# Performance work log

Hardware: AMD Instinct MI355X
Metric: run time of the kernel (lower is better)

## Reference

```python
import jax, jax.numpy as jnp
import numpy as np

B, T_IN, T_OUT, D, M, N = 4, 10, 5, 5, 96, 96
H1 = 64      # hidden dim of deep ConvLSTM layers
ATTN = 32    # attention bottleneck channels
SEL = 0      # selected_dim


def _conv(x, w, b):
    # SAME conv, NCHW / OIHW
    p = (w.shape[-1] - 1) // 2
    y = jax.lax.conv_general_dilated(x, w, (1, 1), [(p, p), (p, p)],
                                     dimension_numbers=('NCHW', 'OIHW', 'NCHW'))
    return y + b[None, :, None, None]


def _cell(xt, h, c, w, b):
    # standard ConvLSTM cell (no peephole): conv over concat(x, h) -> i,f,o,g
    z = _conv(jnp.concatenate([xt, h], axis=1), w, b)
    i, f, o, g = jnp.split(z, 4, axis=1)
    c = jax.nn.sigmoid(f) * c + jax.nn.sigmoid(i) * jnp.tanh(g)
    h = jax.nn.sigmoid(o) * jnp.tanh(c)
    return h, c


def setup_inputs() -> dict:
    key = jax.random.key(0)
    ks = jax.random.split(key, 12)
    w = lambda k, s: jax.random.normal(k, s, jnp.float32) * 0.05
    z = lambda n: jnp.zeros((n,), jnp.float32)
    return {
        'x': jax.random.normal(ks[0], (B, T_IN, D, M, N), jnp.float32),
        # encoder ConvLSTM cells: hidden dims [1, H1, H1]
        'enc_w0': w(ks[1], (4 * 1, D + 1, 3, 3)), 'enc_b0': z(4 * 1),
        'enc_w1': w(ks[2], (4 * H1, 1 + H1, 3, 3)), 'enc_b1': z(4 * H1),
        'enc_w2': w(ks[3], (4 * H1, H1 + H1, 3, 3)), 'enc_b2': z(4 * H1),
        # decoder ConvLSTM cells: hidden dims [H1, H1, 1]
        'dec_w0': w(ks[4], (4 * H1, 1 + H1, 3, 3)), 'dec_b0': z(4 * H1),
        'dec_w1': w(ks[5], (4 * H1, H1 + H1, 3, 3)), 'dec_b1': z(4 * H1),
        'dec_w2': w(ks[6], (4 * 1, H1 + 1, 3, 3)), 'dec_b2': z(4 * 1),
        # input attention (DA-RNN style with convs): e_k = v(tanh(Wi*x_k + Wh*[h;c]))
        'attn_wi': w(ks[7], (ATTN, T_IN, 3, 3)), 'attn_bi': z(ATTN),
        'attn_wh': w(ks[8], (ATTN, 2, 3, 3)), 'attn_bh': z(ATTN),
        'attn_wv': w(ks[9], (1, ATTN, 3, 3)), 'attn_bv': z(1),
        # temporal_cnn: Conv2d(1 + window_in, 1, kernel_size=1) + ReLU
        'tcnn_w': w(ks[10], (1, T_IN + 1, 1, 1)), 'tcnn_b': z(1),
    }


def reference(x, enc_w0, enc_b0, enc_w1, enc_b1, enc_w2, enc_b2,
              dec_w0, dec_b0, dec_w1, dec_b1, dec_w2, dec_b2,
              attn_wi, attn_bi, attn_wh, attn_bh, attn_wv, attn_bv,
              tcnn_w, tcnn_b):
    b = x.shape[0]

    def attn_reweight(xs, h, c):
        # xs: (b, t, d, m, n); hidden term shared across the d channels
        hid_e = _conv(jnp.concatenate([h, c], axis=1), attn_wh, attn_bh)
        def per_k(xk):  # (b, t, m, n): time-as-channels
            e = jnp.tanh(_conv(xk, attn_wi, attn_bi) + hid_e)
            return _conv(e, attn_wv, attn_bv)[:, 0]  # (b, m, n)
        alpha = jax.vmap(per_k, in_axes=2, out_axes=1)(xs)  # (b, d, m, n)
        ea = jnp.exp(alpha)
        return xs * (ea / jnp.max(ea))[:, None]  # global-max normalization

    def run_layer(xs, h, c, w, bb):
        def step(carry, xt):
            hh, cc = _cell(xt, carry[0], carry[1], w, bb)
            return (hh, cc), hh
        (h, c), hs = jax.lax.scan(step, (h, c), jnp.swapaxes(xs, 0, 1))
        return jnp.swapaxes(hs, 0, 1), (h, c)

    # ---------- encoder ----------
    h0 = jnp.zeros((b, 1, M, N), x.dtype); c0 = jnp.zeros_like(h0)
    def enc0_step(carry, t):
        xs, h, c = carry
        xs = attn_reweight(xs, h, c)  # re-weight whole sequence each step
        xt = jax.lax.dynamic_index_in_dim(xs, t, axis=1, keepdims=False)
        h, c = _cell(xt, h, c, enc_w0, enc_b0)
        return (xs, h, c), h
    (_, h0, c0), hs0 = jax.lax.scan(enc0_step, (x, h0, c0), jnp.arange(T_IN))
    out0 = jnp.swapaxes(hs0, 0, 1)  # (b, T_IN, 1, m, n)

    h1 = jnp.zeros((b, H1, M, N), x.dtype); c1 = jnp.zeros_like(h1)
    out1, (h1, c1) = run_layer(out0, h1, c1, enc_w1, enc_b1)
    h2 = jnp.zeros((b, H1, M, N), x.dtype); c2 = jnp.zeros_like(h2)
    out2, (h2, c2) = run_layer(out1, h2, c2, enc_w2, enc_b2)

    # ---------- decoder (encoder states reversed) ----------
    dec_in = jnp.zeros((b, T_OUT, 1, M, N), x.dtype)
    d0, _ = run_layer(dec_in, h2, c2, dec_w0, dec_b0)
    d1, _ = run_layer(d0, h1, c1, dec_w1, dec_b1)

    y_prev = x[:, :, SEL]  # (b, T_IN, m, n): selected variable, time-as-channels
    def dec2_step(carry, xt):
        h, c, yp = carry
        h, c = _cell(xt, h, c, dec_w2, dec_b2)          # (b, 1, m, n)
        ycat = jnp.concatenate([yp, h], axis=1)         # (b, T_IN+1, m, n)
        h = jax.nn.relu(_conv(ycat, tcnn_w, tcnn_b))    # temporal 1x1 CNN readout
        return (h, c, ycat[:, 1:]), h
    _, hs = jax.lax.scan(dec2_step, (h0, c0, y_prev), jnp.swapaxes(d1, 0, 1))
    return jnp.swapaxes(hs, 0, 1)  # (b, T_OUT, 1, m, n)
```

## Files before the change

kernel.cpp:

```cpp
#include <hip/hip_runtime.h>


#define PIX  9216
#define NB   4
#define TIN  10
#define TOUT 5
#define ND   5
#define HID  64

typedef __attribute__((ext_vector_type(8))) short bf16x8;
typedef __attribute__((ext_vector_type(4))) float f32x4;

__device__ __forceinline__ float sigmf_(float x) { return 1.0f / (1.0f + __expf(-x)); }
__device__ __forceinline__ float tanhf_(float x) { return 1.0f - 2.0f / (__expf(2.0f * x) + 1.0f); }
__device__ __forceinline__ unsigned short f2bf(float f) {
    unsigned u = __float_as_uint(f);
    unsigned r = u + 0x7FFFu + ((u >> 16) & 1u);
    return (unsigned short)(r >> 16);
}
__device__ __forceinline__ float bf2f(unsigned short u) {
    return __uint_as_float(((unsigned)u) << 16);
}
__device__ __forceinline__ unsigned fmap_(float f) {
    unsigned u = __float_as_uint(f);
    return (u & 0x80000000u) ? ~u : (u | 0x80000000u);
}
__device__ __forceinline__ float funmap_(unsigned v) {
    return __uint_as_float((v & 0x80000000u) ? (v ^ 0x80000000u) : ~v);
}
__device__ __forceinline__ void gload_lds16(const void* g, void* l) {
    __builtin_amdgcn_global_load_lds(
        (const __attribute__((address_space(1))) void*)g,
        (__attribute__((address_space(3))) void*)l, 16, 0, 0);
}

template <int NCH>
__device__ __forceinline__ void
cell64_body(char* smem, int bid,
            const unsigned short* __restrict__ inP,
            const unsigned short* __restrict__ wP,
            const float* __restrict__ bias,
            const float* cprev, float* cout,
            const float* __restrict__ zeropg,
            unsigned short* __restrict__ d1, int d1_coff, int d1_ncg,
            unsigned short* __restrict__ d2, int d2_coff, int d2_ncg)
{
    const int lane = threadIdx.x;
    const int wv   = threadIdx.y;
    const int tid  = wv * 64 + lane;
    const int rid = (bid & 7) * 48 + (bid >> 3);
    const int y = rid % 96, b = rid / 96;
    const int l15 = lane & 15, l4 = lane >> 4;
    const int NCG = NCH * 4;

    const int scg  = tid & 3;
    const int spr0 = tid >> 2;

    auto stage = [&](char* buf, int cc) {
#pragma unroll
        for (int i = 0; i < 5; ++i) {
            int pr = spr0 + i * 64;
            int r = pr / 98;
            int p = pr - r * 98;
            int gy = y - 1 + r, gx = p - 1;
            const void* g = (const void*)zeropg;
            if (pr < 294 && (unsigned)gy < 96u && (unsigned)gx < 96u) {
                int cg = scg ^ ((p >> 1) & 3);
                g = (const void*)(inP + (((size_t)(b * NCG + cc * 4 + cg) * 9216
                                          + gy * 96 + gx) << 3));
            }
            gload_lds16(g, buf + i * 4096 + wv * 1024);
        }
    };

    f32x4 acc[4][6] = {};
    bf16x8 af[2][4];

#pragma unroll
    for (int g = 0; g < 4; ++g)
        af[0][g] = *(const bf16x8*)(wP
            + ((size_t)(0 * NCH + 0) * 256 + g * 64 + wv * 16 + l15) * 32 + l4 * 8);

    stage(smem, 0);
    __syncthreads();
#pragma unroll
    for (int cc = 0; cc < NCH; ++cc) {
        if (cc + 1 < NCH) stage(smem + ((cc + 1) & 1) * 20480, cc + 1);
        const char* buf = smem + (cc & 1) * 20480;
#pragma unroll
        for (int tap = 0; tap < 9; ++tap) {
            const int T = cc * 9 + tap;
            if (T + 1 < NCH * 9) {
                const int cc2 = (T + 1) / 9, tap2 = (T + 1) % 9;
#pragma unroll
                for (int g = 0; g < 4; ++g)
                    af[(T + 1) & 1][g] = *(const bf16x8*)(wP
                        + ((size_t)(tap2 * NCH + cc2) * 256 + g * 64 + wv * 16 + l15) * 32 + l4 * 8);
            }
            const int ky = tap / 3, kx = tap % 3;
            bf16x8 bk[6];
#pragma unroll
            for (int k = 0; k < 6; ++k) {
                int p = k * 16 + kx + l15;
                int slot = l4 ^ ((p >> 1) & 3);
                bk[k] = *(const bf16x8*)(buf + (ky * 98 + p) * 64 + slot * 16);
            }
            __builtin_amdgcn_s_setprio(1);
#pragma unroll
            for (int g = 0; g < 4; ++g)
#pragma unroll
                for (int k = 0; k < 6; ++k)
                    acc[g][k] = __builtin_amdgcn_mfma_f32_16x16x32_bf16(
                        af[T & 1][g], bk[k], acc[g][k], 0, 0, 0);
            __builtin_amdgcn_s_setprio(0);
        }
        if (cc + 1 < NCH) __syncthreads();
    }

#pragma unroll
    for (int r = 0; r < 4; ++r) {
        int hc = wv * 16 + l4 * 4 + r;
        float bi = bias[hc], bff = bias[64 + hc];
        float bo = bias[128 + hc], bg = bias[192 + hc];
#pragma unroll
        for (int k = 0; k < 6; ++k) {
            int px = k * 16 + l15;
            int gpix = y * 96 + px;
            float ii = sigmf_(acc[0][k][r] + bi);
            float ff = sigmf_(acc[1][k][r] + bff);
            float oo = sigmf_(acc[2][k][r] + bo);
            float gg = tanhf_(acc[3][k][r] + bg);
            int cidx = (b * HID + hc) * 9216 + gpix;
            float cn = ff * cprev[cidx] + ii * gg;
            cout[cidx] = cn;
            unsigned short hb = f2bf(oo * tanhf_(cn));
            int ch1 = d1_coff + hc;
            d1[((size_t)(b * d1_ncg + (ch1 >> 3)) * 9216 + gpix) * 8 + (ch1 & 7)] = hb;
            if (d2) {
                int ch2 = d2_coff + hc;
                d2[((size_t)(b * d2_ncg + (ch2 >> 3)) * 9216 + gpix) * 8 + (ch2 & 7)] = hb;
            }
        }
    }
}

__device__ __forceinline__ void
attnE_body(char* smem, int aid,
           const unsigned short* __restrict__ xsp, const unsigned short* __restrict__ wiP,
           const float* __restrict__ h0, const float* __restrict__ c0,
           const float* __restrict__ wh, const float* __restrict__ bh,
           const float* __restrict__ bi, unsigned short* __restrict__ eP)
{
    float* heS = (float*)smem;
    const int lane = threadIdx.x, wvid = threadIdx.y;
    const int tile = aid % 36, k = (aid / 36) % 5, bb = aid / 180;
    const int l15 = lane & 15, l4 = lane >> 4;
    const int tid = wvid * 64 + lane;

    {
        int p = tile * 256 + tid;
        int y = p / 96, x = p - y * 96;
        float hv9[9], cv9[9];
        const float* hp = h0 + bb * PIX;
        const float* cp = c0 + bb * PIX;
#pragma unroll
        for (int t9 = 0; t9 < 9; ++t9) {
            int gy = y + t9 / 3 - 1, gx = x + t9 % 3 - 1;
            bool ok = (unsigned)gy < 96u && (unsigned)gx < 96u;
            hv9[t9] = ok ? hp[gy * 96 + gx] : 0.0f;
            cv9[t9] = ok ? cp[gy * 96 + gx] : 0.0f;
        }
#pragma unroll
        for (int ch = 0; ch < 32; ++ch) {
            float a = bi[ch] + bh[ch];
#pragma unroll
            for (int t9 = 0; t9 < 9; ++t9) {
                a = fmaf(wh[(ch * 2 + 0) * 9 + t9], hv9[t9], a);
                a = fmaf(wh[(ch * 2 + 1) * 9 + t9], cv9[t9], a);
            }
            heS[tid * 33 + ch] = a;
        }
    }

    bf16x8 af[5][2];
#pragma unroll
    for (int j = 0; j < 5; ++j)
#pragma unroll
        for (int m = 0; m < 2; ++m)
            af[j][m] = *(const bf16x8*)(wiP + ((size_t)(j * 32 + m * 16 + l15)) * 32 + l4 * 8);

    const unsigned short* xb = xsp + (size_t)(bb * ND + k) * PIX * 16;
    const int p0 = tile * 256 + wvid * 64;

    f32x4 acc[4][2] = {};
#pragma unroll
    for (int nf = 0; nf < 4; ++nf) {
        int p = p0 + nf * 16 + l15;
        int y = p / 96, x = p - y * 96;
#pragma unroll
        for (int j = 0; j < 5; ++j) {
            int tp = 2 * j + (l4 >> 1);
            bf16x8 bk = { 0, 0, 0, 0, 0, 0, 0, 0 };
            if (tp < 9) {
                int gy = y + tp / 3 - 1, gx = x + tp % 3 - 1;
                if ((unsigned)gy < 96u && (unsigned)gx < 96u)
                    bk = *(const bf16x8*)(xb + ((size_t)(gy * 96 + gx)) * 16 + (l4 & 1) * 8);
            }
            acc[nf][0] = __builtin_amdgcn_mfma_f32_16x16x32_bf16(af[j][0], bk, acc[nf][0], 0, 0, 0);
            acc[nf][1] = __builtin_amdgcn_mfma_f32_16x16x32_bf16(af[j][1], bk, acc[nf][1], 0, 0, 0);
        }
    }

    __syncthreads();

#pragma unroll
    for (int nf = 0; nf < 4; ++nf) {
        int p = p0 + nf * 16 + l15;
        int pl = wvid * 64 + nf * 16 + l15;
        const float* hrow = &heS[pl * 33];
#pragma unroll
        for (int m = 0; m < 2; ++m) {
            ushort4 o;
            o.x = f2bf(tanhf_(acc[nf][m][0] + hrow[m * 16 + l4 * 4 + 0]));
            o.y = f2bf(tanhf_(acc[nf][m][1] + hrow[m * 16 + l4 * 4 + 1]));
            o.z = f2bf(tanhf_(acc[nf][m][2] + hrow[m * 16 + l4 * 4 + 2]));
            o.w = f2bf(tanhf_(acc[nf][m][3] + hrow[m * 16 + l4 * 4 + 3]));
            *(ushort4*)(eP + ((size_t)(bb * ND + k) * PIX + p) * 32 + m * 16 + l4 * 4) = o;
        }
    }
}

__device__ __forceinline__ void
alpha_body(char* smem, int aid,
           const unsigned short* __restrict__ eP, const float* __restrict__ wvv,
           const float* __restrict__ bv, float* __restrict__ alpha,
           unsigned* __restrict__ msl)
{
    const int tid = threadIdx.y * 64 + threadIdx.x;
    const int tile = aid % 36, k = (aid / 36) % 5, bb = aid / 180;
    int p = tile * 256 + tid;
    int y = p / 96, x = p - y * 96;
    const unsigned short* eb = eP + (size_t)(bb * ND + k) * PIX * 32;
    float acc = bv[0];
#pragma unroll
    for (int ky = 0; ky < 3; ++ky) {
        int gy = y + ky - 1;
        if ((unsigned)gy >= 96u) continue;
#pragma unroll
        for (int kx = 0; kx < 3; ++kx) {
            int gx = x + kx - 1;
            if ((unsigned)gx >= 96u) continue;
            int tap = ky * 3 + kx;
            const unsigned short* ee = eb + ((size_t)(gy * 96 + gx)) * 32;
#pragma unroll
            for (int cg = 0; cg < 4; ++cg) {
                bf16x8 ev = *(const bf16x8*)(ee + cg * 8);
#pragma unroll
                for (int jj = 0; jj < 8; ++jj)
                    acc = fmaf(wvv[(cg * 8 + jj) * 9 + tap], bf2f((unsigned short)ev[jj]), acc);
            }
        }
    }
    alpha[(size_t)(bb * ND + k) * PIX + p] = acc;

    float* s = (float*)smem;
    s[tid] = acc;
    __syncthreads();
    for (int st = 128; st > 0; st >>= 1) {
        if (tid < st) s[tid] = fmaxf(s[tid], s[tid + st]);
        __syncthreads();
    }
    if (tid == 0) atomicMax(msl, fmap_(s[0]));
}

__device__ __forceinline__ void
dec2_body(int did,
          const unsigned short* __restrict__ inP, int ncg, int cgbase,
          const float* __restrict__ hprev, const float* cprev,
          const unsigned short* __restrict__ wm, const float* __restrict__ w2,
          const float* __restrict__ bias,
          const float* __restrict__ tw, const float* __restrict__ tb,
          const float* __restrict__ yprev,
          float* __restrict__ ynext, float* __restrict__ hcarry,
          float* __restrict__ outp, float* cout)
{
    const int wv = threadIdx.y, lane = threadIdx.x;
    const int l15 = lane & 15, l4 = lane >> 4;
    const int bx = did % 144, b = did / 144;
    const int p0 = (bx * 4 + wv) * 16;
    const int y = p0 / 96, xbase = p0 - y * 96;
    const int x = xbase + l15;

    f32x4 acc = {0.f, 0.f, 0.f, 0.f};
#pragma unroll
    for (int ky = 0; ky < 3; ++ky) {
        int gy = y + ky - 1;
        bool oky = (unsigned)gy < 96u;
#pragma unroll
        for (int kx = 0; kx < 3; ++kx) {
            const int tap = ky * 3 + kx;
            int gx = x + kx - 1;
            bool ok = oky && ((unsigned)gx < 96u);
#pragma unroll
            for (int cc = 0; cc < 2; ++cc) {
                bf16x8 a = *(const bf16x8*)(wm + ((size_t)(tap * 2 + cc) * 16 + l15) * 32 + l4 * 8);
                bf16x8 bk = { 0, 0, 0, 0, 0, 0, 0, 0 };
                if (ok)
                    bk = *(const bf16x8*)(inP + ((size_t)(b * ncg + cgbase + cc * 4 + l4) * 9216
                                                 + gy * 96 + gx) * 8);
                acc = __builtin_amdgcn_mfma_f32_16x16x32_bf16(a, bk, acc, 0, 0, 0);
            }
        }
    }

    if (l4 == 0) {
        int px = p0 + l15;
        float aI = acc[0] + bias[0];
        float aF = acc[1] + bias[1];
        float aO = acc[2] + bias[2];
        float aG = acc[3] + bias[3];
        const float* hp = hprev + b * PIX;
#pragma unroll
        for (int ky = 0; ky < 3; ++ky) {
            int gy = y + ky - 1;
            if ((unsigned)gy >= 96u) continue;
#pragma unroll
            for (int kx = 0; kx < 3; ++kx) {
                int gx = x + kx - 1;
                if ((unsigned)gx >= 96u) continue;
                int tap = ky * 3 + kx;
                float hv = hp[gy * 96 + gx];
                aI = fmaf(w2[(0 * 65 + 64) * 9 + tap], hv, aI);
                aF = fmaf(w2[(1 * 65 + 64) * 9 + tap], hv, aF);
                aO = fmaf(w2[(2 * 65 + 64) * 9 + tap], hv, aO);
                aG = fmaf(w2[(3 * 65 + 64) * 9 + tap], hv, aG);
            }
        }
        int idx = b * PIX + px;
        float cn = sigmf_(aF) * cprev[idx] + sigmf_(aI) * tanhf_(aG);
        cout[idx] = cn;
        float h = sigmf_(aO) * tanhf_(cn);

        float a2 = tb[0];
#pragma unroll
        for (int c2 = 0; c2 < TIN; ++c2)
            a2 = fmaf(tw[c2], yprev[(size_t)(b * TIN + c2) * PIX + px], a2);
        a2 = fmaf(tw[TIN], h, a2);
        float o = fmaxf(a2, 0.0f);
        outp[(size_t)b * TOUT * PIX + px] = o;
#pragma unroll
        for (int c2 = 0; c2 < TIN - 1; ++c2)
            ynext[(size_t)(b * TIN + c2) * PIX + px] = yprev[(size_t)(b * TIN + c2 + 1) * PIX + px];
        ynext[(size_t)(b * TIN + 9) * PIX + px] = h;
        hcarry[idx] = o;
    }
}

template <int NCH, bool ATTN>
__global__ void __launch_bounds__(256, 2)
mk_cell_attnE(const unsigned short* __restrict__ inP, const unsigned short* __restrict__ wP,
              const float* __restrict__ bias, const float* cprev, float* cout,
              const float* __restrict__ zeropg,
              unsigned short* __restrict__ d1, int d1_coff, int d1_ncg,
              unsigned short* __restrict__ d2, int d2_coff, int d2_ncg,
              const unsigned short* __restrict__ xsp, const unsigned short* __restrict__ wiP,
              const float* __restrict__ h0, const float* __restrict__ c0,
              const float* __restrict__ wh, const float* __restrict__ bh,
              const float* __restrict__ bi, unsigned short* __restrict__ eP)
{
    __shared__ __align__(16) char smem[40960];
    if (blockIdx.x < 384)
        cell64_body<NCH>(smem, blockIdx.x, inP, wP, bias, cprev, cout, zeropg,
                         d1, d1_coff, d1_ncg, d2, d2_coff, d2_ncg);
    else if (ATTN)
        attnE_body(smem, blockIdx.x - 384, xsp, wiP, h0, c0, wh, bh, bi, eP);
}

template <int NCH, bool ATTN>
__global__ void __launch_bounds__(256, 2)
mk_cell_alpha(const unsigned short* __restrict__ inP, const unsigned short* __restrict__ wP,
              const float* __restrict__ bias, const float* cprev, float* cout,
              const float* __restrict__ zeropg,
              unsigned short* __restrict__ d1, int d1_coff, int d1_ncg,
              unsigned short* __restrict__ d2, int d2_coff, int d2_ncg,
              const unsigned short* __restrict__ eP, const float* __restrict__ wvv,
              const float* __restrict__ bv, float* __restrict__ alpha,
              unsigned* __restrict__ msl)
{
    __shared__ __align__(16) char smem[40960];
    if (blockIdx.x < 384)
        cell64_body<NCH>(smem, blockIdx.x, inP, wP, bias, cprev, cout, zeropg,
                         d1, d1_coff, d1_ncg, d2, d2_coff, d2_ncg);
    else if (ATTN)
        alpha_body(smem, blockIdx.x - 384, eP, wvv, bv, alpha, msl);
}

template <bool HAS0, bool HAS2>
__global__ void __launch_bounds__(256, 2)
mk_dec(const unsigned short* __restrict__ d1in, const unsigned short* __restrict__ wpd1,
       const float* __restrict__ b1, float* c1, unsigned short* __restrict__ d1out,
       const float* __restrict__ zeropg,
       const unsigned short* __restrict__ d0in, const unsigned short* __restrict__ wpd0,
       const float* __restrict__ b0, float* c2, unsigned short* __restrict__ d0out,
       unsigned short* __restrict__ d1next,
       const unsigned short* __restrict__ d2in,
       const float* __restrict__ hprev, float* c0,
       const unsigned short* __restrict__ wd2m, const float* __restrict__ w2,
       const float* __restrict__ b2,
       const float* __restrict__ tw, const float* __restrict__ tb,
       const float* __restrict__ yprev, float* __restrict__ ynext,
       float* __restrict__ hcarry, float* __restrict__ outp)
{
    __shared__ __align__(16) char smem[40960];
    if (blockIdx.x < 384) {
        cell64_body<4>(smem, blockIdx.x, d1in, wpd1, b1, c1, c1, zeropg,
                       d1out, 64, 16, nullptr, 0, 0);
    } else if (blockIdx.x < 768) {
        if (HAS0)
            cell64_body<2>(smem, blockIdx.x - 384, d0in, wpd0, b0, c2, c2, zeropg,
                           d0out, 0, 8, d1next, 0, 16);
    } else {
        if (HAS2)
            dec2_body(blockIdx.x - 768, d2in, 16, 8, hprev, c0, wd2m, w2, b2,
                      tw, tb, yprev, ynext, hcarry, outp, c0);
    }
}

template <int NCH>
__global__ void __launch_bounds__(256, 2)
cell_k(const unsigned short* __restrict__ inP, const unsigned short* __restrict__ wP,
       const float* __restrict__ bias, const float* cprev, float* cout,
       const float* __restrict__ zeropg,
       unsigned short* __restrict__ d1, int d1_coff, int d1_ncg,
       unsigned short* __restrict__ d2, int d2_coff, int d2_ncg)
{
    __shared__ __align__(16) char smem[40960];
    cell64_body<NCH>(smem, blockIdx.x, inP, wP, bias, cprev, cout, zeropg,
                     d1, d1_coff, d1_ncg, d2, d2_coff, d2_ncg);
}

__global__ void __launch_bounds__(256)
dec2_k(const unsigned short* __restrict__ d2in, const float* __restrict__ hprev,
       float* c0, const unsigned short* __restrict__ wd2m, const float* __restrict__ w2,
       const float* __restrict__ b2, const float* __restrict__ tw, const float* __restrict__ tb,
       const float* __restrict__ yprev, float* __restrict__ ynext,
       float* __restrict__ hcarry, float* __restrict__ outp)
{
    dec2_body(blockIdx.x, d2in, 16, 8, hprev, c0, wd2m, w2, b2,
              tw, tb, yprev, ynext, hcarry, outp, c0);
}

__global__ void __launch_bounds__(256)
attn_e_k(const unsigned short* __restrict__ xsp, const unsigned short* __restrict__ wiP,
         const float* __restrict__ h0, const float* __restrict__ c0,
         const float* __restrict__ wh, const float* __restrict__ bh,
         const float* __restrict__ bi, unsigned short* __restrict__ eP)
{
    __shared__ __align__(16) char smem[33792];
    attnE_body(smem, blockIdx.x, xsp, wiP, h0, c0, wh, bh, bi, eP);
}

__global__ void __launch_bounds__(256)
alpha_k(const unsigned short* __restrict__ eP, const float* __restrict__ wvv,
        const float* __restrict__ bv, float* __restrict__ alpha, unsigned* __restrict__ msl)
{
    __shared__ __align__(16) char smem[1024];
    alpha_body(smem, blockIdx.x, eP, wvv, bv, alpha, msl);
}

__global__ void __launch_bounds__(256)
prep_kernel(const float* __restrict__ enc_w1, const float* __restrict__ enc_w2,
            const float* __restrict__ dec_w0, const float* __restrict__ dec_w1,
            const float* __restrict__ dec_w2, const float* __restrict__ attn_wi,
            const float* __restrict__ x,
            unsigned short* __restrict__ wpe1, unsigned short* __restrict__ wpe2,
            unsigned short* __restrict__ wpd0, unsigned short* __restrict__ wpd1,
            unsigned short* __restrict__ wd2m, unsigned short* __restrict__ wiP,
            unsigned short* __restrict__ xsp, float* __restrict__ yp)
{
    int gid = blockIdx.x;
    auto wpack = [&](const float* w, unsigned short* wp, int WCIN, int NCH,
                     int coff, int climit, int base) {
        int idx = (gid - base) * 256 + threadIdx.x;
        if (idx >= 9 * NCH * 256 * 32) return;
        int k = idx & 31;
        int ocp = (idx >> 5) & 255;
        int rest = idx >> 13;
        int cc = rest % NCH, tap = rest / NCH;
        int hc = ocp >> 2, gate = ocp & 3;
        int c = cc * 32 + k;
        float v = 0.0f;
        if (c < climit) v = w[((gate * 64 + hc) * WCIN + (c + coff)) * 9 + tap];
        wp[idx] = f2bf(v);
    };
    if (gid < 864) { wpack(enc_w1, wpe1, 65, 3, 0, 65, 0); return; }
    if (gid < 2016) { wpack(enc_w2, wpe2, 128, 4, 0, 128, 864); return; }
    if (gid < 2592) { wpack(dec_w0, wpd0, 65, 2, 1, 64, 2016); return; }
    if (gid < 3744) { wpack(dec_w1, wpd1, 128, 4, 0, 128, 2592); return; }
    if (gid < 3780) {
        int idx = (gid - 3744) * 256 + threadIdx.x;
        if (idx < 9 * 2 * 16 * 32) {
            int k = idx & 31;
            int oc = (idx >> 5) & 15;
            int cc = (idx >> 9) & 1;
            int tap = idx >> 10;
            float v = 0.0f;
            if (oc < 4) v = dec_w2[(oc * 65 + cc * 32 + k) * 9 + tap];
            wd2m[idx] = f2bf(v);
        }
        return;
    }
    if (gid < 3800) {
        int idx = (gid - 3780) * 256 + threadIdx.x;
        if (idx < 5120) {
            int kl = idx & 31, oc = (idx >> 5) & 31, j = idx >> 10;
            int tappos = kl >> 4, ch = kl & 15;
            int tap = 2 * j + tappos;
            float v = 0.0f;
            if (tap < 9 && ch < 10) v = attn_wi[(oc * TIN + ch) * 9 + tap];
            wiP[idx] = f2bf(v);
        }
        return;
    }
    if (gid < 4520) {
        int idx = (gid - 3800) * 256 + threadIdx.x;
        int p = idx % PIX;
        int q = idx / PIX;
        int d = q % ND, bb = q / ND;
        unsigned short tmp[16];
#pragma unroll
        for (int t = 0; t < TIN; ++t)
            tmp[t] = f2bf(x[((size_t)(bb * TIN + t) * ND + d) * PIX + p]);
#pragma unroll
        for (int t = TIN; t < 16; ++t) tmp[t] = 0;
        uint4* dst = (uint4*)(xsp + (size_t)idx * 16);
        dst[0] = *(uint4*)&tmp[0];
        dst[1] = *(uint4*)&tmp[8];
        return;
    }
    {
        int idx = (gid - 4520) * 256 + threadIdx.x;
        int p = idx % PIX;
        int q = idx / PIX;
        yp[idx] = x[(size_t)(q * ND + 0) * PIX + p];
    }
}


__global__ void __launch_bounds__(256)
small_cell5(const float* __restrict__ xs_t,
            const float* __restrict__ hprev, const float* cprev,
            const float* __restrict__ w, const float* __restrict__ bias,
            float* __restrict__ hout, float* cout,
            unsigned short* __restrict__ pk, int ncg)
{
    __shared__ float z[4][64];
    const int pxl = threadIdx.x & 63, gate = threadIdx.x >> 6;
    const int p = blockIdx.x * 64 + pxl, bb = blockIdx.y;
    const int y = p / 96, x = p - y * 96;
    float acc = bias[gate];
#pragma unroll
    for (int cin = 0; cin < 6; ++cin) {
        const float* src = (cin < 5) ? (xs_t + (bb * TIN * ND + cin) * PIX)
                                     : (hprev + bb * PIX);
        const float* wp = w + (gate * 6 + cin) * 9;
#pragma unroll
        for (int ky = 0; ky < 3; ++ky) {
            int gy = y + ky - 1;
            if ((unsigned)gy >= 96u) continue;
#pragma unroll
            for (int kx = 0; kx < 3; ++kx) {
                int gx = x + kx - 1;
                if ((unsigned)gx >= 96u) continue;
                acc = fmaf(wp[ky * 3 + kx], src[gy * 96 + gx], acc);
            }
        }
    }
    z[gate][pxl] = acc;
    __syncthreads();
    if (threadIdx.x < 64) {
        int pp = blockIdx.x * 64 + threadIdx.x;
        int idx = bb * PIX + pp;
        float cn = sigmf_(z[1][threadIdx.x]) * cprev[idx]
                 + sigmf_(z[0][threadIdx.x]) * tanhf_(z[3][threadIdx.x]);
        cout[idx] = cn;
        float h = sigmf_(z[2][threadIdx.x]) * tanhf_(cn);
        hout[idx] = h;
        pk[((size_t)(bb * ncg) * 9216 + pp) * 8] = f2bf(h);
    }
}

__global__ void scale_pack_kernel(float* __restrict__ xs, unsigned short* __restrict__ xsp,
                                  const float* __restrict__ alpha,
                                  const unsigned* __restrict__ msl)
{
    int idx = blockIdx.x * 256 + threadIdx.x;
    int p = idx % PIX;
    int q = idx / PIX;
    int d = q % ND, bb = q / ND;
    float mval = funmap_(msl[0]);
    float w = __expf(alpha[idx] - mval);
    unsigned short tmp[16];
#pragma unroll
    for (int t = 0; t < TIN; ++t) {
        size_t xi = ((size_t)(bb * TIN + t) * ND + d) * PIX + p;
        float v = xs[xi] * w;
        xs[xi] = v;
        tmp[t] = f2bf(v);
    }
#pragma unroll
    for (int t = TIN; t < 16; ++t) tmp[t] = 0;
    uint4* dst = (uint4*)(xsp + (size_t)idx * 16);
    dst[0] = *(uint4*)&tmp[0];
    dst[1] = *(uint4*)&tmp[8];
}

extern "C" void kernel_launch(void* const* d_in, const int* in_sizes, int n_in,
                              void* d_out, int out_size, void* d_ws, size_t ws_size,
                              hipStream_t stream)
{
    const float* x       = (const float*)d_in[0];
    const float* enc_w0  = (const float*)d_in[1];
    const float* enc_b0  = (const float*)d_in[2];
    const float* enc_w1  = (const float*)d_in[3];
    const float* enc_b1  = (const float*)d_in[4];
    const float* enc_w2  = (const float*)d_in[5];
    const float* enc_b2  = (const float*)d_in[6];
    const float* dec_w0  = (const float*)d_in[7];
    const float* dec_b0  = (const float*)d_in[8];
    const float* dec_w1  = (const float*)d_in[9];
    const float* dec_b1  = (const float*)d_in[10];
    const float* dec_w2  = (const float*)d_in[11];
    const float* dec_b2  = (const float*)d_in[12];
    const float* attn_wi = (const float*)d_in[13];
    const float* attn_bi = (const float*)d_in[14];
    const float* attn_wh = (const float*)d_in[15];
    const float* attn_bh = (const float*)d_in[16];
    const float* attn_wv = (const float*)d_in[17];
    const float* attn_bv = (const float*)d_in[18];
    const float* tcnn_w  = (const float*)d_in[19];
    const float* tcnn_b  = (const float*)d_in[20];
    float* out = (float*)d_out;

    char* cur = (char*)d_ws;
    auto alloc = [&](size_t bytes) { char* p = cur; cur += (bytes + 255) & ~(size_t)255; return p; };
    float* xs   = (float*)alloc((size_t)NB * TIN * ND * PIX * 4);
    float* alp  = (float*)alloc((size_t)NB * ND * PIX * 4);
    float* ypa  = (float*)alloc((size_t)NB * TIN * PIX * 4);
    float* ypb  = (float*)alloc((size_t)NB * TIN * PIX * 4);
    unsigned short* wpe1 = (unsigned short*)alloc((size_t)9 * 3 * 256 * 32 * 2);
    unsigned short* wpe2 = (unsigned short*)alloc((size_t)9 * 4 * 256 * 32 * 2);
    unsigned short* wpd0 = (unsigned short*)alloc((size_t)9 * 2 * 256 * 32 * 2);
    unsigned short* wpd1 = (unsigned short*)alloc((size_t)9 * 4 * 256 * 32 * 2);
    unsigned short* wd2m = (unsigned short*)alloc((size_t)9 * 2 * 16 * 32 * 2);
    unsigned short* xsp  = (unsigned short*)alloc((size_t)NB * ND * PIX * 16 * 2);
    unsigned short* wiP  = (unsigned short*)alloc(5120 * 2);
    unsigned short* eP   = (unsigned short*)alloc((size_t)NB * ND * PIX * 32 * 2);
    char* zbeg = cur;
    float* h0a  = (float*)alloc(NB * PIX * 4);
    float* h0b  = (float*)alloc(NB * PIX * 4);
    float* c0   = (float*)alloc(NB * PIX * 4);
    float* c1   = (float*)alloc((size_t)NB * HID * PIX * 4);
    float* c2   = (float*)alloc((size_t)NB * HID * PIX * 4);
    const size_t IN1_B = (size_t)NB * 12 * PIX * 8 * 2;
    const size_t IN2_B = (size_t)NB * 16 * PIX * 8 * 2;
    unsigned short* In1a = (unsigned short*)alloc(IN1_B);
    unsigned short* In1b = (unsigned short*)alloc(IN1_B);
    unsigned short* In2a = (unsigned short*)alloc(IN2_B);
    unsigned short* In2b = (unsigned short*)alloc(IN2_B);
    unsigned* mslot = (unsigned*)alloc(256);
    float* zeropg = (float*)alloc(256);
    char* zend = cur;

    hipMemcpyAsync(xs, x, (size_t)NB * TIN * ND * PIX * 4, hipMemcpyDeviceToDevice, stream);
    hipMemsetAsync(zbeg, 0, (size_t)(zend - zbeg), stream);
    prep_kernel<<<dim3(5960), 256, 0, stream>>>(enc_w1, enc_w2, dec_w0, dec_w1, dec_w2,
                                                attn_wi, x, wpe1, wpe2, wpd0, wpd1,
                                                wd2m, wiP, xsp, ypa);

    dim3 blk(64, 4);
    float *h0 = h0a, *h0n = h0b;
    unsigned short *i1c = In1a, *i1n = In1b, *i2c = In2a, *i2n = In2b;

    attn_e_k<<<dim3(720), blk, 0, stream>>>(xsp, wiP, h0, c0, attn_wh, attn_bh, attn_bi, eP);
    alpha_k<<<dim3(720), blk, 0, stream>>>(eP, attn_wv, attn_bv, alp, mslot + 0);
    scale_pack_kernel<<<dim3(720), 256, 0, stream>>>(xs, xsp, alp, mslot + 0);
    small_cell5<<<dim3(144, NB), 256, 0, stream>>>(xs + 0, h0, c0, enc_w0, enc_b0,
                                                   h0n, c0, i1c, 12);
    { float* tmp = h0; h0 = h0n; h0n = tmp; }

    for (int t = 0; t < TIN; ++t) {
        const bool hn = (t < TIN - 1);
        unsigned short* e1d1 = hn ? i1n : In2a;
        int e1o = hn ? 1 : 64;
        int e1n = hn ? 12 : 16;
        unsigned short* e2d1 = hn ? i2n : In1a;
        int e2o = hn ? 64 : 0;
        int e2n = hn ? 16 : 8;
        int grid = 384 + (hn ? 720 : 0);

        if (hn)
            mk_cell_attnE<3, true><<<dim3(grid), blk, 0, stream>>>(
                i1c, wpe1, enc_b1, c1, c1, zeropg, e1d1, e1o, e1n, i2c, 0, 16,
                xsp, wiP, h0, c0, attn_wh, attn_bh, attn_bi, eP);
        else
            mk_cell_attnE<3, false><<<dim3(grid), blk, 0, stream>>>(
                i1c, wpe1, enc_b1, c1, c1, zeropg, e1d1, e1o, e1n, i2c, 0, 16,
                xsp, wiP, h0, c0, attn_wh, attn_bh, attn_bi, eP);

        if (hn)
            mk_cell_alpha<4, true><<<dim3(grid), blk, 0, stream>>>(
                i2c, wpe2, enc_b2, c2, c2, zeropg, e2d1, e2o, e2n, nullptr, 0, 0,
                eP, attn_wv, attn_bv, alp, mslot + t + 1);
        else
            mk_cell_alpha<4, false><<<dim3(grid), blk, 0, stream>>>(
                i2c, wpe2, enc_b2, c2, c2, zeropg, e2d1, e2o, e2n, nullptr, 0, 0,
                eP, attn_wv, attn_bv, alp, mslot + t + 1);

        if (hn) {
            scale_pack_kernel<<<dim3(720), 256, 0, stream>>>(xs, xsp, alp, mslot + t + 1);
            small_cell5<<<dim3(144, NB), 256, 0, stream>>>(xs + (size_t)(t + 1) * ND * PIX,
                                                           h0, c0, enc_w0, enc_b0,
                                                           h0n, c0, i1n, 12);
            { float* tmp = h0; h0 = h0n; h0n = tmp; }
        }
        { unsigned short* tmp = i1c; i1c = i1n; i1n = tmp; }
        { unsigned short* tmp = i2c; i2c = i2n; i2n = tmp; }
    }

    float *hc = h0, *hcn = h0n;
    cell_k<2><<<dim3(384), blk, 0, stream>>>(In1a, wpd0, dec_b0, c2, c2, zeropg,
                                             In1b, 0, 8, In2a, 0, 16);
    mk_dec<true, false><<<dim3(768), blk, 0, stream>>>(
        In2a, wpd1, dec_b1, c1, In2b, zeropg,
        In1b, wpd0, dec_b0, c2, In1a, In2b,
        nullptr, nullptr, nullptr, nullptr, nullptr, nullptr, nullptr, nullptr,
        nullptr, nullptr, nullptr, nullptr);
    mk_dec<true, true><<<dim3(1344), blk, 0, stream>>>(
        In2b, wpd1, dec_b1, c1, In2a, zeropg,
        In1a, wpd0, dec_b0, c2, In1b, In2a,
        In2b, hc, c0, wd2m, dec_w2, dec_b2, tcnn_w, tcnn_b,
        ypa, ypb, hcn, out + 0 * PIX);
    mk_dec<true, true><<<dim3(1344), blk, 0, stream>>>(
        In2a, wpd1, dec_b1, c1, In2b, zeropg,
        In1b, wpd0, dec_b0, c2, In1a, In2b,
        In2a, hcn, c0, wd2m, dec_w2, dec_b2, tcnn_w, tcnn_b,
        ypb, ypa, hc, out + 1 * PIX);
    mk_dec<true, true><<<dim3(1344), blk, 0, stream>>>(
        In2b, wpd1, dec_b1, c1, In2a, zeropg,
        In1a, wpd0, dec_b0, c2, In1b, In2a,
        In2b, hc, c0, wd2m, dec_w2, dec_b2, tcnn_w, tcnn_b,
        ypa, ypb, hcn, out + 2 * PIX);
    mk_dec<false, true><<<dim3(1344), blk, 0, stream>>>(
        In2a, wpd1, dec_b1, c1, In2b, zeropg,
        nullptr, nullptr, nullptr, nullptr, nullptr, nullptr,
        In2a, hcn, c0, wd2m, dec_w2, dec_b2, tcnn_w, tcnn_b,
        ypb, ypa, hc, out + 3 * PIX);
    dec2_k<<<dim3(576), blk, 0, stream>>>(In2b, hc, c0, wd2m, dec_w2, dec_b2,
                                          tcnn_w, tcnn_b, ypa, ypb, hcn, out + 4 * PIX);
}
```

Baseline: 1.285 ms.

## Fuse attention scaling with first ConvLSTM cell and deepen weight prefetch

Merges the attention-weighted input scaling/packing kernel and the layer-0 ConvLSTM cell into a single launch. Input buffers are ping-ponged so the cell blocks can recompute the scaled input from the unscaled copy without waiting on the scaling blocks. The MFMA conv loop also prefetches weight fragments two taps ahead using a triple buffer instead of one tap ahead. The aim is to cut launch and serialization overhead per timestep and hide weight-load latency, at the cost of redundant exp computations, extra workspace and more registers.

```diff
diff --git a/kernel.cpp b/kernel.cpp
--- a/kernel.cpp
+++ b/kernel.cpp
@@ -74,12 +74,14 @@
     };
 
     f32x4 acc[4][6] = {};
-    bf16x8 af[2][4];
-
-#pragma unroll
-    for (int g = 0; g < 4; ++g)
-        af[0][g] = *(const bf16x8*)(wP
-            + ((size_t)(0 * NCH + 0) * 256 + g * 64 + wv * 16 + l15) * 32 + l4 * 8);
+    bf16x8 af[3][4];
+
+#pragma unroll
+    for (int t0 = 0; t0 < 2; ++t0)
+#pragma unroll
+        for (int g = 0; g < 4; ++g)
+            af[t0][g] = *(const bf16x8*)(wP
+                + ((size_t)(t0 * NCH + 0) * 256 + g * 64 + wv * 16 + l15) * 32 + l4 * 8);
 
     stage(smem, 0);
     __syncthreads();
@@ -90,11 +92,12 @@
 #pragma unroll
         for (int tap = 0; tap < 9; ++tap) {
             const int T = cc * 9 + tap;
-            if (T + 1 < NCH * 9) {
-                const int cc2 = (T + 1) / 9, tap2 = (T + 1) % 9;
+            const int Tp = T + 2;
+            if (Tp < NCH * 9) {
+                const int cc2 = Tp / 9, tap2 = Tp % 9;
 #pragma unroll
                 for (int g = 0; g < 4; ++g)
-                    af[(T + 1) & 1][g] = *(const bf16x8*)(wP
+                    af[Tp % 3][g] = *(const bf16x8*)(wP
                         + ((size_t)(tap2 * NCH + cc2) * 256 + g * 64 + wv * 16 + l15) * 32 + l4 * 8);
             }
             const int ky = tap / 3, kx = tap % 3;
@@ -111,7 +114,7 @@
 #pragma unroll
                 for (int k = 0; k < 6; ++k)
                     acc[g][k] = __builtin_amdgcn_mfma_f32_16x16x32_bf16(
-                        af[T & 1][g], bk[k], acc[g][k], 0, 0, 0);
+                        af[T % 3][g], bk[k], acc[g][k], 0, 0, 0);
             __builtin_amdgcn_s_setprio(0);
         }
         if (cc + 1 < NCH) __syncthreads();
@@ -393,6 +396,83 @@
                          d1, d1_coff, d1_ncg, d2, d2_coff, d2_ncg);
     else if (ATTN)
         alpha_body(smem, blockIdx.x - 384, eP, wvv, bv, alpha, msl);
+}
+
+__global__ void __launch_bounds__(256)
+mk_scale_small5(const float* __restrict__ xs_cur, float* __restrict__ xs_nxt,
+                unsigned short* __restrict__ xsp,
+                const float* __restrict__ alpha, const unsigned* __restrict__ msl,
+                int ts,
+                const float* __restrict__ h0in, const float* cprev,
+                const float* __restrict__ w, const float* __restrict__ bias,
+                float* __restrict__ h0out, float* cout,
+                unsigned short* __restrict__ pk, int ncg)
+{
+    __shared__ float z[4][64];
+    const int bid = blockIdx.x;
+    const float mval = funmap_(msl[0]);
+    if (bid < 720) {
+        int idx = bid * 256 + threadIdx.x;
+        int p = idx % PIX;
+        int q = idx / PIX;
+        int d = q % ND, bb = q / ND;
+        float wgt = __expf(alpha[idx] - mval);
+        unsigned short tmp[16];
+#pragma unroll
+        for (int t = 0; t < TIN; ++t) {
+            size_t xi = ((size_t)(bb * TIN + t) * ND + d) * PIX + p;
+            float v = xs_cur[xi] * wgt;
+            xs_nxt[xi] = v;
+            tmp[t] = f2bf(v);
+        }
+#pragma unroll
+        for (int t = TIN; t < 16; ++t) tmp[t] = 0;
+        uint4* dst = (uint4*)(xsp + (size_t)idx * 16);
+        dst[0] = *(uint4*)&tmp[0];
+        dst[1] = *(uint4*)&tmp[8];
+    } else {
+        int bid2 = bid - 720;
+        int bx = bid2 % 144, bb = bid2 / 144;
+        const int pxl = threadIdx.x & 63, gate = threadIdx.x >> 6;
+        const int p = bx * 64 + pxl;
+        const int y = p / 96, x = p - y * 96;
+        float acc = bias[gate];
+#pragma unroll
+        for (int cin = 0; cin < 6; ++cin) {
+            const float* wp = w + (gate * 6 + cin) * 9;
+#pragma unroll
+            for (int ky = 0; ky < 3; ++ky) {
+                int gy = y + ky - 1;
+                if ((unsigned)gy >= 96u) continue;
+#pragma unroll
+                for (int kx = 0; kx < 3; ++kx) {
+                    int gx = x + kx - 1;
+                    if ((unsigned)gx >= 96u) continue;
+                    int np = gy * 96 + gx;
+                    float v;
+                    if (cin < 5) {
+                        float raw = xs_cur[((size_t)(bb * TIN + ts) * ND + cin) * PIX + np];
+                        v = raw * __expf(alpha[(size_t)(bb * ND + cin) * PIX + np] - mval);
+                    } else {
+                        v = h0in[bb * PIX + np];
+                    }
+                    acc = fmaf(wp[ky * 3 + kx], v, acc);
+                }
+            }
+        }
+        z[gate][pxl] = acc;
+        __syncthreads();
+        if (threadIdx.x < 64) {
+            int pp = bx * 64 + threadIdx.x;
+            int idx = bb * PIX + pp;
+            float cn = sigmf_(z[1][threadIdx.x]) * cprev[idx]
+                     + sigmf_(z[0][threadIdx.x]) * tanhf_(z[3][threadIdx.x]);
+            cout[idx] = cn;
+            float h = sigmf_(z[2][threadIdx.x]) * tanhf_(cn);
+            h0out[idx] = h;
+            pk[((size_t)(bb * ncg) * 9216 + pp) * 8] = f2bf(h);
+        }
+    }
 }
 
 template <bool HAS0, bool HAS2>
@@ -546,75 +626,6 @@
     }
 }
 
-
-__global__ void __launch_bounds__(256)
-small_cell5(const float* __restrict__ xs_t,
-            const float* __restrict__ hprev, const float* cprev,
-            const float* __restrict__ w, const float* __restrict__ bias,
-            float* __restrict__ hout, float* cout,
-            unsigned short* __restrict__ pk, int ncg)
-{
-    __shared__ float z[4][64];
-    const int pxl = threadIdx.x & 63, gate = threadIdx.x >> 6;
-    const int p = blockIdx.x * 64 + pxl, bb = blockIdx.y;
-    const int y = p / 96, x = p - y * 96;
-    float acc = bias[gate];
-#pragma unroll
-    for (int cin = 0; cin < 6; ++cin) {
-        const float* src = (cin < 5) ? (xs_t + (bb * TIN * ND + cin) * PIX)
-                                     : (hprev + bb * PIX);
-        const float* wp = w + (gate * 6 + cin) * 9;
-#pragma unroll
-        for (int ky = 0; ky < 3; ++ky) {
-            int gy = y + ky - 1;
-            if ((unsigned)gy >= 96u) continue;
-#pragma unroll
-            for (int kx = 0; kx < 3; ++kx) {
-                int gx = x + kx - 1;
-                if ((unsigned)gx >= 96u) continue;
-                acc = fmaf(wp[ky * 3 + kx], src[gy * 96 + gx], acc);
-            }
-        }
-    }
-    z[gate][pxl] = acc;
-    __syncthreads();
-    if (threadIdx.x < 64) {
-        int pp = blockIdx.x * 64 + threadIdx.x;
-        int idx = bb * PIX + pp;
-        float cn = sigmf_(z[1][threadIdx.x]) * cprev[idx]
-                 + sigmf_(z[0][threadIdx.x]) * tanhf_(z[3][threadIdx.x]);
-        cout[idx] = cn;
-        float h = sigmf_(z[2][threadIdx.x]) * tanhf_(cn);
-        hout[idx] = h;
-        pk[((size_t)(bb * ncg) * 9216 + pp) * 8] = f2bf(h);
-    }
-}
-
-__global__ void scale_pack_kernel(float* __restrict__ xs, unsigned short* __restrict__ xsp,
-                                  const float* __restrict__ alpha,
-                                  const unsigned* __restrict__ msl)
-{
-    int idx = blockIdx.x * 256 + threadIdx.x;
-    int p = idx % PIX;
-    int q = idx / PIX;
-    int d = q % ND, bb = q / ND;
-    float mval = funmap_(msl[0]);
-    float w = __expf(alpha[idx] - mval);
-    unsigned short tmp[16];
-#pragma unroll
-    for (int t = 0; t < TIN; ++t) {
-        size_t xi = ((size_t)(bb * TIN + t) * ND + d) * PIX + p;
-        float v = xs[xi] * w;
-        xs[xi] = v;
-        tmp[t] = f2bf(v);
-    }
-#pragma unroll
-    for (int t = TIN; t < 16; ++t) tmp[t] = 0;
-    uint4* dst = (uint4*)(xsp + (size_t)idx * 16);
-    dst[0] = *(uint4*)&tmp[0];
-    dst[1] = *(uint4*)&tmp[8];
-}
-
 extern "C" void kernel_launch(void* const* d_in, const int* in_sizes, int n_in,
                               void* d_out, int out_size, void* d_ws, size_t ws_size,
                               hipStream_t stream)
@@ -644,7 +655,8 @@
 
     char* cur = (char*)d_ws;
     auto alloc = [&](size_t bytes) { char* p = cur; cur += (bytes + 255) & ~(size_t)255; return p; };
-    float* xs   = (float*)alloc((size_t)NB * TIN * ND * PIX * 4);
+    float* xsA  = (float*)alloc((size_t)NB * TIN * ND * PIX * 4);
+    float* xsB  = (float*)alloc((size_t)NB * TIN * ND * PIX * 4);
     float* alp  = (float*)alloc((size_t)NB * ND * PIX * 4);
     float* ypa  = (float*)alloc((size_t)NB * TIN * PIX * 4);
     float* ypb  = (float*)alloc((size_t)NB * TIN * PIX * 4);
@@ -672,7 +684,7 @@
     float* zeropg = (float*)alloc(256);
     char* zend = cur;
 
-    hipMemcpyAsync(xs, x, (size_t)NB * TIN * ND * PIX * 4, hipMemcpyDeviceToDevice, stream);
+    hipMemcpyAsync(xsA, x, (size_t)NB * TIN * ND * PIX * 4, hipMemcpyDeviceToDevice, stream);
     hipMemsetAsync(zbeg, 0, (size_t)(zend - zbeg), stream);
     prep_kernel<<<dim3(5960), 256, 0, stream>>>(enc_w1, enc_w2, dec_w0, dec_w1, dec_w2,
                                                 attn_wi, x, wpe1, wpe2, wpd0, wpd1,
@@ -680,14 +692,15 @@
 
     dim3 blk(64, 4);
     float *h0 = h0a, *h0n = h0b;
+    float *xc = xsA, *xn = xsB;
     unsigned short *i1c = In1a, *i1n = In1b, *i2c = In2a, *i2n = In2b;
 
     attn_e_k<<<dim3(720), blk, 0, stream>>>(xsp, wiP, h0, c0, attn_wh, attn_bh, attn_bi, eP);
     alpha_k<<<dim3(720), blk, 0, stream>>>(eP, attn_wv, attn_bv, alp, mslot + 0);
-    scale_pack_kernel<<<dim3(720), 256, 0, stream>>>(xs, xsp, alp, mslot + 0);
-    small_cell5<<<dim3(144, NB), 256, 0, stream>>>(xs + 0, h0, c0, enc_w0, enc_b0,
-                                                   h0n, c0, i1c, 12);
+    mk_scale_small5<<<dim3(1296), 256, 0, stream>>>(xc, xn, xsp, alp, mslot + 0, 0,
+                                                    h0, c0, enc_w0, enc_b0, h0n, c0, i1c, 12);
     { float* tmp = h0; h0 = h0n; h0n = tmp; }
+    { float* tmp = xc; xc = xn; xn = tmp; }
 
     for (int t = 0; t < TIN; ++t) {
         const bool hn = (t < TIN - 1);
@@ -718,11 +731,11 @@
                 eP, attn_wv, attn_bv, alp, mslot + t + 1);
 
         if (hn) {
-            scale_pack_kernel<<<dim3(720), 256, 0, stream>>>(xs, xsp, alp, mslot + t + 1);
-            small_cell5<<<dim3(144, NB), 256, 0, stream>>>(xs + (size_t)(t + 1) * ND * PIX,
-                                                           h0, c0, enc_w0, enc_b0,
-                                                           h0n, c0, i1n, 12);
+            mk_scale_small5<<<dim3(1296), 256, 0, stream>>>(xc, xn, xsp, alp, mslot + t + 1,
+                                                            t + 1, h0, c0, enc_w0, enc_b0,
+                                                            h0n, c0, i1n, 12);
             { float* tmp = h0; h0 = h0n; h0n = tmp; }
+            { float* tmp = xc; xc = xn; xn = tmp; }
         }
         { unsigned short* tmp = i1c; i1c = i1n; i1n = tmp; }
         { unsigned short* tmp = i2c; i2c = i2n; i2n = tmp; }
```

Result: no change. 1.270 ms (-1.2%).
